# Optimization experiments

Measured on AMD Instinct MI355X. Metric: run time of the kernel, lower is better.

## Reference

```python
import jax, jax.numpy as jnp
import numpy as np

IN_MODES = (4, 4, 8, 8, 4)
OUT_MODES = (4, 4, 8, 8, 4)
RANKS = (1, 8, 8, 8, 8, 1)
N_TOKENS = 8192


def setup_inputs() -> dict:
    key = jax.random.key(0)
    ks = jax.random.split(key, 7)
    inp = jax.random.normal(ks[0], (N_TOKENS, int(np.prod(IN_MODES))), dtype=jnp.float32)
    cores = []
    for i in range(5):
        shape = (IN_MODES[i], RANKS[i], RANKS[i + 1], OUT_MODES[i])
        # kaiming-uniform-like small init to keep the 5-core chain numerically tame
        fan_in = shape[0] * shape[1] * shape[2]
        bound = float(np.sqrt(3.0 / fan_in))
        cores.append(jax.random.uniform(ks[i + 1], shape, minval=-bound, maxval=bound, dtype=jnp.float32))
    biases = jax.random.uniform(ks[6], (int(np.prod(OUT_MODES)),), minval=-0.05, maxval=0.05, dtype=jnp.float32)
    return {
        "input": inp,
        "core0": cores[0], "core1": cores[1], "core2": cores[2],
        "core3": cores[3], "core4": cores[4],
        "biases": biases,
    }


def reference(input, core0, core1, core2, core3, core4, biases):
    # reshape tokens into the 5 input modes: [N, a, b, c, d, e]
    x = input.reshape((-1,) + IN_MODES)
    # TT contraction. Original einsum has no '->'; free indices h (ranks[0]=1)
    # and m (ranks[5]=1) are size-1 boundary ranks, so summing them out here is
    # equivalent to the original reshape-squeeze.
    out = jnp.einsum(
        'nabcde,ahiv,bijw,cjkx,dkly,elmz->nvwxyz',
        x, core0, core1, core2, core3, core4,
        optimize='optimal',
    )
    out = out.reshape(-1, int(np.prod(OUT_MODES)))
    return out + biases
```

## Files before the change

### kernel.cpp

```cpp
#include <hip/hip_runtime.h>

#define DIM 4096

typedef __bf16 bf16x8 __attribute__((ext_vector_type(8)));
typedef float floatx4 __attribute__((ext_vector_type(4)));

__device__ __forceinline__ void async_ld16(void* lds, const void* g) {
  __builtin_amdgcn_global_load_lds(
      (const __attribute__((address_space(1))) unsigned int*)g,
      (__attribute__((address_space(3))) unsigned int*)lds, 16, 0, 0);
}

__global__ void build_k(const float* __restrict__ c0, const float* __restrict__ c1,
                        const float* __restrict__ c2, const float* __restrict__ c3,
                        const float* __restrict__ c4,
                        float* __restrict__ K012, float* __restrict__ K34T) {
  const int bid = blockIdx.x, tid = threadIdx.x;
  if (bid < 512) {
    __shared__ float K01s[128];
    const int abc = bid >> 2;
    const int ab = abc >> 3, c = abc & 7;
    if (tid < 128) {
      const int a = ab >> 2, b = ab & 3;
      const int j = tid >> 4, vw = tid & 15, v = vw >> 2, w = vw & 3;
      float s = 0.f;
#pragma unroll
      for (int i = 0; i < 8; ++i)
        s += c0[a * 32 + i * 4 + v] * c1[b * 256 + i * 32 + j * 4 + w];
      K01s[tid] = s;
    }
    __syncthreads();
    const int t = bid * 256 + tid;
    const int vwx = t & 127, k = (t >> 7) & 7;
    const int vw = vwx >> 3, xx = vwx & 7;
    float s = 0.f;
#pragma unroll
    for (int j = 0; j < 8; ++j)
      s += K01s[j * 16 + vw] * c2[c * 512 + j * 64 + k * 8 + xx];
    K012[t] = s;
  } else {
    const int u = (bid - 512) * 256 + tid;
    const int yz = u & 31, kk = (u >> 5) & 7, de = u >> 8;
    const int d = de >> 2, e = de & 3, y = yz >> 2, z = yz & 3;
    float s = 0.f;
#pragma unroll
    for (int l = 0; l < 8; ++l)
      s += c3[d * 512 + kk * 64 + l * 8 + y] * c4[e * 32 + l * 4 + z];
    K34T[kk * 1024 + yz * 32 + de] = s;
  }
}

__global__ void build_wt_conv(const float* __restrict__ K012, const float* __restrict__ K34T,
                              __bf16* __restrict__ WT,
                              const float* __restrict__ X, __bf16* __restrict__ Xb) {
  const int bid = blockIdx.x, tid = threadIdx.x;
  if (bid < 8192) {
    const long t = (long)bid * 256 + tid;
    const long e8 = t * 8;
    const int in = (int)(e8 & 4095), o = (int)(e8 >> 12);
    const int de0 = in & 31, abc = in >> 5;
    const int yz = o & 31, vwx = o >> 5;
    const float* kp = K012 + abc * 1024 + vwx;
    const float* vp = K34T + yz * 32 + de0;
    float s[8] = {};
#pragma unroll
    for (int k = 0; k < 8; ++k) {
      const float a = kp[k * 128];
      const float4 v0 = *(const float4*)(vp + k * 1024);
      const float4 v1 = *(const float4*)(vp + k * 1024 + 4);
      s[0] += a * v0.x; s[1] += a * v0.y; s[2] += a * v0.z; s[3] += a * v0.w;
      s[4] += a * v1.x; s[5] += a * v1.y; s[6] += a * v1.z; s[7] += a * v1.w;
    }
    bf16x8 w;
#pragma unroll
    for (int d = 0; d < 8; ++d) w[d] = (__bf16)s[d];
    ((bf16x8*)WT)[t] = w;
  } else {
    const long t = (long)(bid - 8192) * 256 + tid;
    const float4 a = ((const float4*)X)[t * 2];
    const float4 b = ((const float4*)X)[t * 2 + 1];
    bf16x8 w;
    w[0] = (__bf16)a.x; w[1] = (__bf16)a.y; w[2] = (__bf16)a.z; w[3] = (__bf16)a.w;
    w[4] = (__bf16)b.x; w[5] = (__bf16)b.y; w[6] = (__bf16)b.z; w[7] = (__bf16)b.w;
    ((bf16x8*)Xb)[t] = w;
  }
}


#define G_BAR1() do { __builtin_amdgcn_s_barrier(); \
                      asm volatile("s_waitcnt lgkmcnt(0)" ::: "memory"); \
                      __builtin_amdgcn_sched_barrier(0); } while (0)
#define G_BAR2() do { __builtin_amdgcn_s_barrier(); \
                      __builtin_amdgcn_sched_barrier(0); } while (0)
#define G_VM6()  asm volatile("s_waitcnt vmcnt(6)" ::: "memory")

#define G_STA(p, h, koff) do { \
  async_ld16(&As[p][(h) * 128][0] + ldsq[0], agp[0] + (h) * 524288 + (koff)); \
  async_ld16(&As[p][(h) * 128][0] + ldsq[1], agp[1] + (h) * 524288 + (koff)); } while (0)
#define G_STB(p, h, koff) do { \
  async_ld16(&Bs[p][(h) * 128][0] + ldsq[0], bgp[0] + (h) * 524288 + (koff)); \
  async_ld16(&Bs[p][(h) * 128][0] + ldsq[1], bgp[1] + (h) * 524288 + (koff)); } while (0)

#define G_LDA(p, mh) do { \
  _Pragma("unroll") for (int fi = 0; fi < 4; ++fi) { \
    const int row = ((mh) * 8 + 2 * fi + wm) * 16 + lm; \
    _Pragma("unroll") for (int kh = 0; kh < 2; ++kh) \
      af[fi][kh] = *(const bf16x8*)&As[p][row][((kh * 4 + kq) ^ (row & 7)) * 8]; \
  } } while (0)
#define G_LDB(p, nh) do { \
  _Pragma("unroll") for (int gi = 0; gi < 2; ++gi) { \
    const int g = (nh) * 2 + gi; \
    const int row = (4 * g + wn) * 16 + lm; \
    _Pragma("unroll") for (int kh = 0; kh < 2; ++kh) \
      bfv[g][kh] = *(const bf16x8*)&Bs[p][row][((kh * 4 + kq) ^ (row & 7)) * 8]; \
  } } while (0)

#define G_MMA(mh, nh) do { \
  __builtin_amdgcn_s_setprio(1); \
  _Pragma("unroll") for (int fi = 0; fi < 4; ++fi) \
  _Pragma("unroll") for (int gi = 0; gi < 2; ++gi) \
  _Pragma("unroll") for (int kh = 0; kh < 2; ++kh) \
    acc[(mh) * 4 + fi][(nh) * 2 + gi] = __builtin_amdgcn_mfma_f32_16x16x32_bf16( \
        af[fi][kh], bfv[(nh) * 2 + gi][kh], acc[(mh) * 4 + fi][(nh) * 2 + gi], 0, 0, 0); \
  __builtin_amdgcn_s_setprio(0); } while (0)

__global__ __launch_bounds__(512, 2) void gemm_8ph(const __bf16* __restrict__ A,
                                                   const __bf16* __restrict__ WT,
                                                   const float* __restrict__ bias,
                                                   float* __restrict__ C) {
  __shared__ __bf16 As[2][256][64];
  __shared__ __bf16 Bs[2][256][64];

  const int tid = threadIdx.x;
  const int gb = (blockIdx.x & 7) * 64 + (blockIdx.x >> 3);
  const int m0 = (gb >> 4) * 256;
  const int n0 = (gb & 15) * 256;

  const int wave = tid >> 6, lane = tid & 63;
  const int wm = wave & 1, wn = wave >> 1;
  const int lm = lane & 15, kq = lane >> 4;

  floatx4 acc[8][4] = {};
  bf16x8 af[4][2], bfv[4][2];

  const __bf16* agp[2];
  const __bf16* bgp[2];
  int ldsq[2];
#pragma unroll
  for (int j = 0; j < 2; ++j) {
    const int q = tid + j * 512;
    const int r = q >> 3, pc = q & 7;
    const int c = pc ^ (r & 7);
    ldsq[j] = q * 8;
    agp[j] = A + (long)(m0 + r) * DIM + c * 8;
    bgp[j] = WT + (long)(n0 + r) * DIM + c * 8;
  }

  G_STA(0, 0, 0); G_STB(0, 0, 0); G_STB(0, 1, 0); G_STA(0, 1, 0);
  G_STA(1, 0, 64); G_STB(1, 0, 64); G_STB(1, 1, 64);
  G_VM6();
  __builtin_amdgcn_s_barrier();
  __builtin_amdgcn_sched_barrier(0);

#pragma unroll 1
  for (int it = 0; it < 32; ++it) {
    const int kA = (2 * it + 1) * 64;
    int t2 = 2 * it + 2; if (t2 > 63) t2 = 63;
    int t3 = 2 * it + 3; if (t3 > 63) t3 = 63;
    const int kB = t2 * 64, kC = t3 * 64;

    G_LDA(0, 0); G_LDB(0, 0);
    G_STA(1, 1, kA);
    G_BAR1(); G_MMA(0, 0); G_BAR2();

    G_LDB(0, 1);
    G_STA(0, 0, kB);
    G_BAR1(); G_MMA(0, 1); G_BAR2();

    G_LDA(0, 1);
    G_STB(0, 0, kB);
    G_BAR1(); G_MMA(1, 0); G_BAR2();

    G_STB(0, 1, kB);
    G_BAR1(); G_MMA(1, 1);
    G_VM6();
    G_BAR2();

    G_LDA(1, 0); G_LDB(1, 0);
    G_STA(0, 1, kB);
    G_BAR1(); G_MMA(0, 0); G_BAR2();

    G_LDB(1, 1);
    G_STA(1, 0, kC);
    G_BAR1(); G_MMA(0, 1); G_BAR2();

    G_LDA(1, 1);
    G_STB(1, 0, kC);
    G_BAR1(); G_MMA(1, 0); G_BAR2();

    G_STB(1, 1, kC);
    G_BAR1(); G_MMA(1, 1);
    G_VM6();
    G_BAR2();
  }

  float bv[4];
#pragma unroll
  for (int g = 0; g < 4; ++g) bv[g] = bias[n0 + (4 * g + wn) * 16 + lm];
#pragma unroll
  for (int f = 0; f < 8; ++f) {
    const long mr = m0 + (2 * f + wm) * 16 + kq * 4;
#pragma unroll
    for (int g = 0; g < 4; ++g) {
      float* cp = C + mr * DIM + n0 + (4 * g + wn) * 16 + lm;
      cp[0]       = acc[f][g][0] + bv[g];
      cp[DIM]     = acc[f][g][1] + bv[g];
      cp[2 * DIM] = acc[f][g][2] + bv[g];
      cp[3 * DIM] = acc[f][g][3] + bv[g];
    }
  }
}

__global__ __launch_bounds__(256) void gemm_xw(const float* __restrict__ X,
                                               const __bf16* __restrict__ WT,
                                               const float* __restrict__ bias,
                                               float* __restrict__ C) {
  __shared__ __bf16 Asf[128 * 40];
  __shared__ __bf16 Bsf[128 * 32];

  const int tid = threadIdx.x;
  const int n0 = (blockIdx.x & 31) * 128;
  const int m0 = (blockIdx.x >> 5) * 128;

  const int wave = tid >> 6, lane = tid & 63;
  const int wm = (wave >> 1) * 64, wn = (wave & 1) * 64;
  const int lm = lane & 15, kq = lane >> 4;

  floatx4 acc[4][4] = {};

  const int ar = tid >> 1;
  const int ac = (tid & 1) * 16;
  const float* xp = X + (long)(m0 + ar) * DIM + ac;
  __bf16* as_dst = &Asf[ar * 40 + ac];

  const int u0 = tid, u1 = 256 + tid;
  const int r0 = u0 >> 2, r1 = u1 >> 2;
  const int ch0 = (u0 & 3) ^ (r0 & 3), ch1 = (u1 & 3) ^ (r1 & 3);
  const __bf16* wp0 = WT + (long)(n0 + r0) * DIM + ch0 * 8;
  const __bf16* wp1 = WT + (long)(n0 + r1) * DIM + ch1 * 8;

  float4 a0 = *(const float4*)(xp);
  float4 a1 = *(const float4*)(xp + 4);
  float4 a2 = *(const float4*)(xp + 8);
  float4 a3 = *(const float4*)(xp + 12);

#pragma unroll 1
  for (int k0 = 0; k0 < DIM; k0 += 32) {
    async_ld16(&Bsf[u0 * 8], wp0 + k0);
    async_ld16(&Bsf[u1 * 8], wp1 + k0);

    bf16x8 w0, w1;
    w0[0] = (__bf16)a0.x; w0[1] = (__bf16)a0.y; w0[2] = (__bf16)a0.z; w0[3] = (__bf16)a0.w;
    w0[4] = (__bf16)a1.x; w0[5] = (__bf16)a1.y; w0[6] = (__bf16)a1.z; w0[7] = (__bf16)a1.w;
    w1[0] = (__bf16)a2.x; w1[1] = (__bf16)a2.y; w1[2] = (__bf16)a2.z; w1[3] = (__bf16)a2.w;
    w1[4] = (__bf16)a3.x; w1[5] = (__bf16)a3.y; w1[6] = (__bf16)a3.z; w1[7] = (__bf16)a3.w;
    *(bf16x8*)(as_dst) = w0;
    *(bf16x8*)(as_dst + 8) = w1;

    if (k0 + 32 < DIM) {
      a0 = *(const float4*)(xp + k0 + 32);
      a1 = *(const float4*)(xp + k0 + 36);
      a2 = *(const float4*)(xp + k0 + 40);
      a3 = *(const float4*)(xp + k0 + 44);
    }
    __syncthreads();

    bf16x8 afv[4], bfr[4];
#pragma unroll
    for (int mi = 0; mi < 4; ++mi)
      afv[mi] = *(const bf16x8*)&Asf[(wm + mi * 16 + lm) * 40 + kq * 8];
#pragma unroll
    for (int ni = 0; ni < 4; ++ni) {
      int rr = wn + ni * 16 + lm;
      bfr[ni] = *(const bf16x8*)&Bsf[rr * 32 + ((kq ^ (rr & 3)) * 8)];
    }
#pragma unroll
    for (int mi = 0; mi < 4; ++mi)
#pragma unroll
      for (int ni = 0; ni < 4; ++ni)
        acc[mi][ni] = __builtin_amdgcn_mfma_f32_16x16x32_bf16(afv[mi], bfr[ni], acc[mi][ni], 0, 0, 0);
    __syncthreads();
  }

  float bv[4];
#pragma unroll
  for (int ni = 0; ni < 4; ++ni) bv[ni] = bias[n0 + wn + ni * 16 + lm];
#pragma unroll
  for (int mi = 0; mi < 4; ++mi) {
    long mr = m0 + wm + mi * 16 + kq * 4;
#pragma unroll
    for (int ni = 0; ni < 4; ++ni) {
      float* cp = C + mr * DIM + (n0 + wn + ni * 16 + lm);
      cp[0]       = acc[mi][ni][0] + bv[ni];
      cp[DIM]     = acc[mi][ni][1] + bv[ni];
      cp[2 * DIM] = acc[mi][ni][2] + bv[ni];
      cp[3 * DIM] = acc[mi][ni][3] + bv[ni];
    }
  }
}

extern "C" void kernel_launch(void* const* d_in, const int* in_sizes, int n_in,
                              void* d_out, int out_size, void* d_ws, size_t ws_size,
                              hipStream_t stream) {
  const float* x    = (const float*)d_in[0];
  const float* c0   = (const float*)d_in[1];
  const float* c1   = (const float*)d_in[2];
  const float* c2   = (const float*)d_in[3];
  const float* c3   = (const float*)d_in[4];
  const float* c4   = (const float*)d_in[5];
  const float* bias = (const float*)d_in[6];
  float* out = (float*)d_out;

  const size_t XB_SZ = 67108864;
  const size_t WT_SZ = 33554432;
  const size_t K012_SZ = 524288;
  const size_t K34_SZ = 32768;
  char* ws = (char*)d_ws;

  if (ws_size >= XB_SZ + WT_SZ + K012_SZ + K34_SZ) {
    __bf16* Xb  = (__bf16*)ws;
    __bf16* WT  = (__bf16*)(ws + XB_SZ);
    float* K012 = (float*)(ws + XB_SZ + WT_SZ);
    float* K34T = (float*)(ws + XB_SZ + WT_SZ + K012_SZ);

    build_k<<<544, 256, 0, stream>>>(c0, c1, c2, c3, c4, K012, K34T);
    build_wt_conv<<<24576, 256, 0, stream>>>(K012, K34T, WT, x, Xb);
    gemm_8ph<<<512, 512, 0, stream>>>(Xb, WT, bias, out);
  } else {
    __bf16* WT  = (__bf16*)ws;
    float* K012 = (float*)(ws + WT_SZ);
    float* K34T = (float*)(ws + WT_SZ + K012_SZ);

    build_k<<<544, 256, 0, stream>>>(c0, c1, c2, c3, c4, K012, K34T);
    build_wt_conv<<<8192, 256, 0, stream>>>(K012, K34T, WT, x, (__bf16*)nullptr);
    gemm_xw<<<2048, 256, 0, stream>>>(x, WT, bias, out);
  }
}
```

Before: 486.7 us.

## Restructure GEMM main loop into staggered LDS-read/MMA phases with double-buffered B fragments

Rewrites the 8-phase GEMM loop so LDS fragment reads for the next phase are issued before the barrier and overlap the MFMA work of the current phase. B fragments are now held in a two-slot register buffer, and the per-phase lgkmcnt(0) wait plus second barrier are replaced by a single vmcnt wait and barrier per phase. Global-to-LDS stores are also reordered across phases. The aim is to hide LDS read latency behind the matrix instructions and cut barrier overhead. The cost is more complex hazard reasoning and a chance of a read-after-write race on the LDS buffers.

```diff
diff --git a/kernel.cpp b/kernel.cpp
--- a/kernel.cpp
+++ b/kernel.cpp
@@ -87,42 +87,49 @@
 }
 
 
-#define G_BAR1() do { __builtin_amdgcn_s_barrier(); \
-                      asm volatile("s_waitcnt lgkmcnt(0)" ::: "memory"); \
-                      __builtin_amdgcn_sched_barrier(0); } while (0)
-#define G_BAR2() do { __builtin_amdgcn_s_barrier(); \
-                      __builtin_amdgcn_sched_barrier(0); } while (0)
-#define G_VM6()  asm volatile("s_waitcnt vmcnt(6)" ::: "memory")
-
-#define G_STA(p, h, koff) do { \
+#define SB0()  __builtin_amdgcn_sched_barrier(0)
+#define BARO() do { __builtin_amdgcn_s_barrier(); SB0(); } while (0)
+#define ENDPH() do { asm volatile("s_waitcnt vmcnt(6)" ::: "memory"); \
+                     __builtin_amdgcn_s_barrier(); SB0(); } while (0)
+#define P1() __builtin_amdgcn_s_setprio(1)
+#define P0() __builtin_amdgcn_s_setprio(0)
+
+#define STA(p, h, koff) do { \
   async_ld16(&As[p][(h) * 128][0] + ldsq[0], agp[0] + (h) * 524288 + (koff)); \
   async_ld16(&As[p][(h) * 128][0] + ldsq[1], agp[1] + (h) * 524288 + (koff)); } while (0)
-#define G_STB(p, h, koff) do { \
+#define STB(p, h, koff) do { \
   async_ld16(&Bs[p][(h) * 128][0] + ldsq[0], bgp[0] + (h) * 524288 + (koff)); \
   async_ld16(&Bs[p][(h) * 128][0] + ldsq[1], bgp[1] + (h) * 524288 + (koff)); } while (0)
 
-#define G_LDA(p, mh) do { \
-  _Pragma("unroll") for (int fi = 0; fi < 4; ++fi) { \
+#define RDA2(p, mh, f0) do { \
+  _Pragma("unroll") for (int fi = (f0); fi < (f0) + 2; ++fi) { \
     const int row = ((mh) * 8 + 2 * fi + wm) * 16 + lm; \
     _Pragma("unroll") for (int kh = 0; kh < 2; ++kh) \
       af[fi][kh] = *(const bf16x8*)&As[p][row][((kh * 4 + kq) ^ (row & 7)) * 8]; \
   } } while (0)
-#define G_LDB(p, nh) do { \
-  _Pragma("unroll") for (int gi = 0; gi < 2; ++gi) { \
-    const int g = (nh) * 2 + gi; \
-    const int row = (4 * g + wn) * 16 + lm; \
-    _Pragma("unroll") for (int kh = 0; kh < 2; ++kh) \
-      bfv[g][kh] = *(const bf16x8*)&Bs[p][row][((kh * 4 + kq) ^ (row & 7)) * 8]; \
-  } } while (0)
-
-#define G_MMA(mh, nh) do { \
-  __builtin_amdgcn_s_setprio(1); \
+#define RDB1(p, nh, sl, gi) do { \
+  const int row = (4 * ((nh) * 2 + (gi)) + wn) * 16 + lm; \
+  _Pragma("unroll") for (int kh = 0; kh < 2; ++kh) \
+    bs[sl][gi][kh] = *(const bf16x8*)&Bs[p][row][((kh * 4 + kq) ^ (row & 7)) * 8]; \
+  } while (0)
+
+#define MMA8F(sl, mh, nh, f0) do { \
+  _Pragma("unroll") for (int fi = (f0); fi < (f0) + 2; ++fi) \
+  _Pragma("unroll") for (int gi = 0; gi < 2; ++gi) \
+  _Pragma("unroll") for (int kh = 0; kh < 2; ++kh) \
+    acc[(mh) * 4 + fi][(nh) * 2 + gi] = __builtin_amdgcn_mfma_f32_16x16x32_bf16( \
+        af[fi][kh], bs[sl][gi][kh], acc[(mh) * 4 + fi][(nh) * 2 + gi], 0, 0, 0); } while (0)
+#define MMA8G(sl, mh, nh, gi) do { \
+  _Pragma("unroll") for (int fi = 0; fi < 4; ++fi) \
+  _Pragma("unroll") for (int kh = 0; kh < 2; ++kh) \
+    acc[(mh) * 4 + fi][(nh) * 2 + (gi)] = __builtin_amdgcn_mfma_f32_16x16x32_bf16( \
+        af[fi][kh], bs[sl][gi][kh], acc[(mh) * 4 + fi][(nh) * 2 + (gi)], 0, 0, 0); } while (0)
+#define MMA16(sl, mh, nh) do { \
   _Pragma("unroll") for (int fi = 0; fi < 4; ++fi) \
   _Pragma("unroll") for (int gi = 0; gi < 2; ++gi) \
   _Pragma("unroll") for (int kh = 0; kh < 2; ++kh) \
     acc[(mh) * 4 + fi][(nh) * 2 + gi] = __builtin_amdgcn_mfma_f32_16x16x32_bf16( \
-        af[fi][kh], bfv[(nh) * 2 + gi][kh], acc[(mh) * 4 + fi][(nh) * 2 + gi], 0, 0, 0); \
-  __builtin_amdgcn_s_setprio(0); } while (0)
+        af[fi][kh], bs[sl][gi][kh], acc[(mh) * 4 + fi][(nh) * 2 + gi], 0, 0, 0); } while (0)
 
 __global__ __launch_bounds__(512, 2) void gemm_8ph(const __bf16* __restrict__ A,
                                                    const __bf16* __restrict__ WT,
@@ -141,7 +148,7 @@
   const int lm = lane & 15, kq = lane >> 4;
 
   floatx4 acc[8][4] = {};
-  bf16x8 af[4][2], bfv[4][2];
+  bf16x8 af[4][2], bs[2][2][2];
 
   const __bf16* agp[2];
   const __bf16* bgp[2];
@@ -156,52 +163,50 @@
     bgp[j] = WT + (long)(n0 + r) * DIM + c * 8;
   }
 
-  G_STA(0, 0, 0); G_STB(0, 0, 0); G_STB(0, 1, 0); G_STA(0, 1, 0);
-  G_STA(1, 0, 64); G_STB(1, 0, 64); G_STB(1, 1, 64);
-  G_VM6();
+  STB(0, 0, 0); STA(0, 0, 0); STB(0, 1, 0); STA(0, 1, 0); STB(1, 0, 64);
+  asm volatile("s_waitcnt vmcnt(6)" ::: "memory");
   __builtin_amdgcn_s_barrier();
-  __builtin_amdgcn_sched_barrier(0);
+  SB0();
+  RDB1(0, 0, 1, 0); RDB1(0, 0, 1, 1);
 
 #pragma unroll 1
   for (int it = 0; it < 32; ++it) {
-    const int kA = (2 * it + 1) * 64;
+    const int kE1 = (2 * it + 1) * 64;
     int t2 = 2 * it + 2; if (t2 > 63) t2 = 63;
     int t3 = 2 * it + 3; if (t3 > 63) t3 = 63;
-    const int kB = t2 * 64, kC = t3 * 64;
-
-    G_LDA(0, 0); G_LDB(0, 0);
-    G_STA(1, 1, kA);
-    G_BAR1(); G_MMA(0, 0); G_BAR2();
-
-    G_LDB(0, 1);
-    G_STA(0, 0, kB);
-    G_BAR1(); G_MMA(0, 1); G_BAR2();
-
-    G_LDA(0, 1);
-    G_STB(0, 0, kB);
-    G_BAR1(); G_MMA(1, 0); G_BAR2();
-
-    G_STB(0, 1, kB);
-    G_BAR1(); G_MMA(1, 1);
-    G_VM6();
-    G_BAR2();
-
-    G_LDA(1, 0); G_LDB(1, 0);
-    G_STA(0, 1, kB);
-    G_BAR1(); G_MMA(0, 0); G_BAR2();
-
-    G_LDB(1, 1);
-    G_STA(1, 0, kC);
-    G_BAR1(); G_MMA(0, 1); G_BAR2();
-
-    G_LDA(1, 1);
-    G_STB(1, 0, kC);
-    G_BAR1(); G_MMA(1, 0); G_BAR2();
-
-    G_STB(1, 1, kC);
-    G_BAR1(); G_MMA(1, 1);
-    G_VM6();
-    G_BAR2();
+    const int k2 = t2 * 64, k3 = t3 * 64;
+
+    RDA2(0, 0, 0); SB0(); RDA2(0, 0, 2); STA(1, 0, kE1);
+    BARO(); P1(); MMA8F(1, 0, 0, 0); SB0(); MMA8F(1, 0, 0, 2); P0();
+    ENDPH();
+
+    RDB1(0, 1, 0, 0); SB0(); RDB1(0, 1, 0, 1); STB(1, 1, kE1);
+    BARO(); P1(); MMA8G(0, 0, 1, 0); SB0(); MMA8G(0, 0, 1, 1); P0();
+    ENDPH();
+
+    RDA2(0, 1, 0); SB0(); RDA2(0, 1, 2); STA(1, 1, kE1);
+    BARO(); P1(); MMA8F(0, 1, 1, 0); SB0(); MMA8F(0, 1, 1, 2); P0();
+    ENDPH();
+
+    RDB1(1, 0, 0, 0); SB0(); RDB1(1, 0, 0, 1); STB(0, 0, k2);
+    BARO(); P1(); MMA16(1, 1, 0); P0();
+    ENDPH();
+
+    RDA2(1, 0, 0); SB0(); RDA2(1, 0, 2); STA(0, 0, k2);
+    BARO(); P1(); MMA8F(0, 0, 0, 0); SB0(); MMA8F(0, 0, 0, 2); P0();
+    ENDPH();
+
+    RDB1(1, 1, 1, 0); SB0(); RDB1(1, 1, 1, 1); STB(0, 1, k2);
+    BARO(); P1(); MMA8G(1, 0, 1, 0); SB0(); MMA8G(1, 0, 1, 1); P0();
+    ENDPH();
+
+    RDA2(1, 1, 0); SB0(); RDA2(1, 1, 2); STA(0, 1, k2);
+    BARO(); P1(); MMA8F(1, 1, 1, 0); SB0(); MMA8F(1, 1, 1, 2); P0();
+    ENDPH();
+
+    RDB1(0, 0, 1, 0); SB0(); RDB1(0, 0, 1, 1); STB(1, 0, k3);
+    BARO(); P1(); MMA16(0, 1, 0); P0();
+    ENDPH();
   }
 
   float bv[4];
```

Result: slower. 500.4 us (+2.8%).
